# Performance work log

Measured on AMD Instinct MI355X. Metric: run time of the kernel, lower is better.

Reference implementation:

```python
import jax, jax.numpy as jnp
import numpy as np

B, LP, LH, D, H = 32, 1024, 1024, 256, 256

def setup_inputs() -> dict:
    key = jax.random.key(0)
    k1, k2, k3 = jax.random.split(key, 3)
    premises = jax.random.normal(k1, (B, LP, D), dtype=jnp.float32)
    hypotheses = jax.random.normal(k2, (B, LH, D), dtype=jnp.float32)
    W_F = jax.random.normal(k3, (D, H), dtype=jnp.float32) * (1.0 / np.sqrt(D))
    return {"premises": premises, "hypotheses": hypotheses, "W_F": W_F}

def reference(premises, hypotheses, W_F):
    # Tanh-projected features: F_p = tanh(P @ W_F), F_h = tanh(H @ W_F)
    F_p = jnp.tanh(jnp.einsum('bpd,dh->bph', premises, W_F))   # [B,LP,H]
    F_h = jnp.tanh(jnp.einsum('bqd,dh->bqh', hypotheses, W_F)) # [B,LH,H]
    # Alignment scores e_ij = F_p . F_h
    eijs = jnp.einsum('bph,bqh->bpq', F_p, F_h)                # [B,LP,LH]
    # betas: for each premise token, softmax over hypothesis tokens, weighted sum of hypotheses
    betas = jnp.einsum('bpq,bqd->bpd', jax.nn.softmax(eijs, axis=-1), hypotheses)  # [B,LP,D]
    # alphas: for each hypothesis token, softmax over premise tokens, weighted sum of premises
    alphas = jnp.einsum('bqp,bpd->bqd',
                        jax.nn.softmax(jnp.swapaxes(eijs, 1, 2), axis=-1),
                        premises)                                                   # [B,LH,D]
    return betas, alphas
```

## Files before the change

### kernel.cpp

```cpp
#include <hip/hip_runtime.h>

typedef _Float16 f16;
typedef __attribute__((ext_vector_type(4))) _Float16 f16x4;
typedef __attribute__((ext_vector_type(8))) _Float16 f16x8;
typedef __attribute__((ext_vector_type(4))) float f32x4;
typedef __attribute__((ext_vector_type(16))) float f32x16;
typedef unsigned int u32;

#define BB 32
#define LL 1024
#define DD 256

#define VMCNT(N) asm volatile("s_waitcnt vmcnt(" #N ")" ::: "memory")
#define LGKMCNT0 asm volatile("s_waitcnt lgkmcnt(0)" ::: "memory")

__device__ __forceinline__ void async_copy16(const f16* g, f16* l) {
  __builtin_amdgcn_global_load_lds(
      (const __attribute__((address_space(1))) u32*)(const void*)g,
      (__attribute__((address_space(3))) u32*)(void*)l, 16, 0, 0);
}

__device__ __forceinline__ u32 pack_pkrtz(float a, float b) {
  auto pk = __builtin_amdgcn_cvt_pkrtz(a, b);
  u32 w;
  __builtin_memcpy(&w, &pk, 4);
  return w;
}

__global__ __launch_bounds__(256) void transpose_to_f16(
    const float* __restrict__ X0, f16* __restrict__ Y0,
    const float* __restrict__ X1, f16* __restrict__ Y1,
    int L, int D, int nbPerInput) {
  __shared__ float T[64][68];
  const int tid = threadIdx.x;
  int bz = blockIdx.z;
  const float* X = X0;
  f16* Y = Y0;
  int b = bz;
  if (bz >= nbPerInput) { X = X1; Y = Y1; b = bz - nbPerInput; }
  const int l0 = blockIdx.x * 64, d0 = blockIdx.y * 64;
  const size_t baseX = (size_t)b * L * D;
#pragma unroll
  for (int pass = 0; pass < 4; ++pass) {
    int r = (tid >> 4) + pass * 16;
    int c = (tid & 15) * 4;
    float4 v = *(const float4*)&X[baseX + (size_t)(l0 + r) * D + d0 + c];
    *(float4*)&T[r][c] = v;
  }
  __syncthreads();
  const size_t baseY = (size_t)b * D * L;
#pragma unroll
  for (int pass = 0; pass < 2; ++pass) {
    int dr = (tid >> 3) + pass * 32;
    int lc = (tid & 7) * 8;
    f16x8 o;
#pragma unroll
    for (int j = 0; j < 8; ++j) o[j] = (f16)T[lc + j][dr];
    *(f16x8*)&Y[baseY + (size_t)(d0 + dr) * L + l0 + lc] = o;
  }
}

__global__ __launch_bounds__(256, 2) void proj_mfma(
    const float* __restrict__ Pin, const float* __restrict__ Hin,
    const f16* __restrict__ Wt, f16* __restrict__ Fp, f16* __restrict__ Fh,
    f16* __restrict__ Vtp, f16* __restrict__ Vth) {
  __shared__ f16 As[64][258];
  __shared__ f16 Wts[64][258];
  const int tid = threadIdx.x;
  const int wv = tid >> 6, lane = tid & 63;
  const int l32 = lane & 31, half = lane >> 5;
  const int wm = wv >> 1, wn = wv & 1;
  const float* A = blockIdx.z ? Hin : Pin;
  f16* F = blockIdx.z ? Fh : Fp;
  f16* VtO = blockIdx.z ? Vth : Vtp;
  const int m0 = blockIdx.x * 64;

  {
    const int r = tid >> 4;
    const int c4 = (tid & 15) * 4;
#pragma unroll
    for (int p = 0; p < 4; ++p)
#pragma unroll
      for (int ch = 0; ch < 4; ++ch) {
        float4 v =
            *(const float4*)&A[(size_t)(m0 + r + p * 16) * 256 + ch * 64 + c4];
        f16x4 h4;
        h4[0] = (f16)v.x; h4[1] = (f16)v.y; h4[2] = (f16)v.z; h4[3] = (f16)v.w;
        *(f16x4*)&As[r + p * 16][ch * 64 + c4] = h4;
      }
  }
  __syncthreads();

  f16x8 af[16];
#pragma unroll
  for (int ks = 0; ks < 16; ++ks)
    af[ks] = *(const f16x8*)&As[wm * 32 + l32][ks * 16 + half * 8];

  {
    const int dd = tid & 63, lg = tid >> 6;
    const int bI = m0 >> 10, l_base = m0 & 1023;
#pragma unroll
    for (int kc = 0; kc < 4; ++kc) {
      f16* vrow =
          VtO + (size_t)bI * DD * LL + (size_t)(kc * 64 + dd) * LL + l_base;
#pragma unroll
      for (int part = 0; part < 2; ++part) {
        int lo = lg * 16 + part * 8;
        f16x8 ov;
#pragma unroll
        for (int j = 0; j < 8; ++j) ov[j] = As[lo + j][kc * 64 + dd];
        *(f16x8*)&vrow[lo] = ov;
      }
    }
  }

  for (int nc = 0; nc < 4; ++nc) {
    __syncthreads();
#pragma unroll
    for (int pass = 0; pass < 8; ++pass) {
      int row = (tid >> 5) + pass * 8;
      int chunk = tid & 31;
      *(f16x8*)&Wts[row][chunk * 8] =
          *(const f16x8*)&Wt[(size_t)(nc * 64 + row) * 256 + chunk * 8];
    }
    __syncthreads();
    f32x16 acc = (f32x16)(0.f);
#pragma unroll
    for (int ks = 0; ks < 16; ++ks) {
      f16x8 wf = *(const f16x8*)&Wts[wn * 32 + l32][ks * 16 + half * 8];
      acc = __builtin_amdgcn_mfma_f32_32x32x16_f16(af[ks], wf, acc, 0, 0, 0);
    }
#pragma unroll
    for (int r = 0; r < 16; ++r) {
      float x = acc[r];
      float e = __expf(2.f * x);
      float th = 1.f - 2.f / (e + 1.f);
      F[(size_t)(m0 + wm * 32 + (r & 3) + 8 * (r >> 2) + 4 * half) * 256 +
        nc * 64 + wn * 32 + l32] = (f16)th;
    }
  }
}

__global__ __launch_bounds__(256, 2) void flash_mfma(
    const f16* __restrict__ Fpm, const f16* __restrict__ Fhm,
    const f16* __restrict__ Vth, const f16* __restrict__ Vtp,
    float* __restrict__ Out) {
  __shared__ f16 Kf[2][16][512];
  __shared__ f16 Vf[2][16][512];

  const int tid = threadIdx.x;
  const int wv = tid >> 6, lane = tid & 63;
  const int l32 = lane & 31, half = lane >> 5;

  const f16* Fq = Fpm;
  const f16* Fk = Fhm;
  const f16* Vt = Vth;
  float* O = Out;
  if (blockIdx.y) { Fq = Fhm; Fk = Fpm; Vt = Vtp; O = Out + (size_t)BB * LL * DD; }

  const int x = blockIdx.x;
  const int b = ((x & 7) << 2) | (x >> 6);
  const int p0 = ((x >> 3) & 7) * 128 + wv * 32;
  const int p = p0 + l32;

  const f16* Fq_b = Fq + (size_t)b * LL * DD;
  const f16* Fk_b = Fk + (size_t)b * LL * DD;
  const f16* Vt_b = Vt + (size_t)b * DD * LL;

  f16x8 qf[16];
  {
    const f16* qrow = Fq_b + (size_t)p * DD + half * 8;
#pragma unroll
    for (int s = 0; s < 16; ++s) qf[s] = *(const f16x8*)&qrow[s * 16];
  }

  float m_run = -1e30f, l_run = 0.f;
  f32x16 o[8];
#pragma unroll
  for (int t = 0; t < 8; ++t) o[t] = (f32x16)(0.f);

  auto stage = [&](int buf, int q0) {
#pragma unroll
    for (int i = 0; i < 4; ++i) {
      int s = wv * 4 + i;
      async_copy16(Fk_b + (size_t)(q0 + l32) * DD + s * 16 + half * 8,
                   &Kf[buf][s][0]);
    }
#pragma unroll
    for (int i = 0; i < 4; ++i) {
      int v = wv * 4 + i;
      int t = v >> 1, h = v & 1;
      async_copy16(Vt_b + (size_t)(t * 32 + l32) * LL + q0 + h * 16 + half * 8,
                   &Vf[buf][v][0]);
    }
  };

  auto tile_compute = [&](int cur) {
    f32x16 S = (f32x16)(0.f);
    __builtin_amdgcn_s_setprio(1);
#pragma unroll
    for (int s = 0; s < 16; ++s) {
      f16x8 kf = *(const f16x8*)&Kf[cur][s][lane * 8];
      S = __builtin_amdgcn_mfma_f32_32x32x16_f16(kf, qf[s], S, 0, 0, 0);
    }
    __builtin_amdgcn_s_setprio(0);

    float mt = S[0];
#pragma unroll
    for (int r = 1; r < 16; ++r) mt = fmaxf(mt, S[r]);
    mt = fmaxf(mt, __shfl_xor(mt, 32, 64));

    const bool keep = __all((int)(mt - m_run <= 8.0f)) != 0;
    const float mn = keep ? m_run : fmaxf(m_run, mt);
    float pe[16];
    float ts = 0.f;
#pragma unroll
    for (int r = 0; r < 16; ++r) {
      pe[r] = __expf(S[r] - mn);
      ts += pe[r];
    }
    ts += __shfl_xor(ts, 32, 64);
    if (!keep) {
      const float alpha = __expf(m_run - mn);
      l_run *= alpha;
      m_run = mn;
#pragma unroll
      for (int t = 0; t < 8; ++t)
#pragma unroll
        for (int r = 0; r < 16; ++r) o[t][r] *= alpha;
    }
    l_run += ts;

    u32 pw[8];
#pragma unroll
    for (int i = 0; i < 8; ++i) pw[i] = pack_pkrtz(pe[2 * i], pe[2 * i + 1]);
    u32 rc[4];
    {
      u32 s0 = half ? pw[0] : pw[2];
      u32 s1 = half ? pw[1] : pw[3];
      u32 s2 = half ? pw[4] : pw[6];
      u32 s3 = half ? pw[5] : pw[7];
      rc[0] = (u32)__shfl_xor((int)s0, 32, 64);
      rc[1] = (u32)__shfl_xor((int)s1, 32, 64);
      rc[2] = (u32)__shfl_xor((int)s2, 32, 64);
      rc[3] = (u32)__shfl_xor((int)s3, 32, 64);
    }
    f16x8 pf[2];
#pragma unroll
    for (int h = 0; h < 2; ++h) {
      u32 tmp[4];
      tmp[0] = half ? rc[2 * h] : pw[4 * h];
      tmp[1] = half ? rc[2 * h + 1] : pw[4 * h + 1];
      tmp[2] = half ? pw[4 * h + 2] : rc[2 * h];
      tmp[3] = half ? pw[4 * h + 3] : rc[2 * h + 1];
      __builtin_memcpy(&pf[h], tmp, 16);
    }

    __builtin_amdgcn_s_setprio(1);
#pragma unroll
    for (int t = 0; t < 8; ++t) {
      f16x8 v0 = *(const f16x8*)&Vf[cur][t * 2][lane * 8];
      o[t] = __builtin_amdgcn_mfma_f32_32x32x16_f16(v0, pf[0], o[t], 0, 0, 0);
      f16x8 v1 = *(const f16x8*)&Vf[cur][t * 2 + 1][lane * 8];
      o[t] = __builtin_amdgcn_mfma_f32_32x32x16_f16(v1, pf[1], o[t], 0, 0, 0);
    }
    __builtin_amdgcn_s_setprio(0);
  };

  stage(0, 0);
  int cur = 0;
  for (int it = 0; it < 31; ++it) {
    stage(cur ^ 1, (it + 1) * 32);
    VMCNT(8);
    __builtin_amdgcn_sched_barrier(0);
    __builtin_amdgcn_s_barrier();
    tile_compute(cur);
    __builtin_amdgcn_s_barrier();
    cur ^= 1;
  }
  VMCNT(0);
  __builtin_amdgcn_sched_barrier(0);
  __builtin_amdgcn_s_barrier();
  tile_compute(cur);
  __syncthreads();

  const float inv = 1.f / l_run;
  float* Tw = (float*)&Kf[0][0][0] + wv * (32 * 36);
  float* Ob = O + (size_t)b * LL * DD;
#pragma unroll
  for (int t = 0; t < 8; ++t) {
#pragma unroll
    for (int g = 0; g < 4; ++g) {
      int C = 2 * g + half;
      f32x4 v;
      v[0] = o[t][4 * g + 0] * inv;
      v[1] = o[t][4 * g + 1] * inv;
      v[2] = o[t][4 * g + 2] * inv;
      v[3] = o[t][4 * g + 3] * inv;
      *(f32x4*)&Tw[l32 * 36 + C * 4] = v;
    }
    LGKMCNT0;
#pragma unroll
    for (int pass = 0; pass < 4; ++pass) {
      int row = pass * 8 + (lane >> 3);
      int Cr = lane & 7;
      f32x4 v = *(const f32x4*)&Tw[row * 36 + Cr * 4];
      *(f32x4*)&Ob[(size_t)(p0 + row) * DD + t * 32 + Cr * 4] = v;
    }
    LGKMCNT0;
  }
}

extern "C" void kernel_launch(void* const* d_in, const int* in_sizes, int n_in,
                              void* d_out, int out_size, void* d_ws,
                              size_t ws_size, hipStream_t stream) {
  const float* premises = (const float*)d_in[0];
  const float* hypotheses = (const float*)d_in[1];
  const float* W = (const float*)d_in[2];
  float* out = (float*)d_out;

  const size_t MF = (size_t)BB * LL * DD;
  f16* Fp = (f16*)d_ws;
  f16* Fh = Fp + MF;
  f16* Vth = Fh + MF;
  f16* Vtp = Vth + MF;
  f16* Wt = (f16*)((char*)d_out + (size_t)out_size * 4 - 256 * 256 * 2);

  transpose_to_f16<<<dim3(4, 4, 1), 256, 0, stream>>>(W, Wt, W, Wt, 256, 256, 1);
  proj_mfma<<<dim3(512, 1, 2), 256, 0, stream>>>(premises, hypotheses, Wt, Fp,
                                                 Fh, Vtp, Vth);
  flash_mfma<<<dim3(256, 2), 256, 0, stream>>>(Fp, Fh, Vth, Vtp, out);
}
```

Measured before the change: 227.1 us.

## Pre-swizzle projected features and tiled V layout for contiguous async loads

The projection kernel now writes F rows with an XOR swizzle through shared memory. It writes V transposed into per-32-token tiles of 256x32, so the flash kernel can stage whole contiguous 16-byte lanes with global_load_lds and read them bank-conflict-free using matching XOR indices. W is read directly from global memory instead of being staged in LDS, which frees shared memory so occupancy can rise to 3 blocks. The QK product is split into two independent accumulators to shorten the MFMA dependency chain. The costs are extra XOR index arithmetic, uncached global reads of W per wave, and a dependency on both kernels agreeing on the swizzle.

```diff
diff --git a/kernel.cpp b/kernel.cpp
--- a/kernel.cpp
+++ b/kernel.cpp
@@ -60,12 +60,11 @@
   }
 }
 
-__global__ __launch_bounds__(256, 2) void proj_mfma(
+__global__ __launch_bounds__(256, 3) void proj_mfma(
     const float* __restrict__ Pin, const float* __restrict__ Hin,
     const f16* __restrict__ Wt, f16* __restrict__ Fp, f16* __restrict__ Fh,
     f16* __restrict__ Vtp, f16* __restrict__ Vth) {
-  __shared__ f16 As[64][258];
-  __shared__ f16 Wts[64][258];
+  __shared__ f16 As[64][264];
   const int tid = threadIdx.x;
   const int wv = tid >> 6, lane = tid & 63;
   const int l32 = lane & 31, half = lane >> 5;
@@ -79,14 +78,14 @@
     const int r = tid >> 4;
     const int c4 = (tid & 15) * 4;
 #pragma unroll
-    for (int p = 0; p < 4; ++p)
+    for (int pp = 0; pp < 4; ++pp)
 #pragma unroll
       for (int ch = 0; ch < 4; ++ch) {
         float4 v =
-            *(const float4*)&A[(size_t)(m0 + r + p * 16) * 256 + ch * 64 + c4];
+            *(const float4*)&A[(size_t)(m0 + r + pp * 16) * 256 + ch * 64 + c4];
         f16x4 h4;
         h4[0] = (f16)v.x; h4[1] = (f16)v.y; h4[2] = (f16)v.z; h4[3] = (f16)v.w;
-        *(f16x4*)&As[r + p * 16][ch * 64 + c4] = h4;
+        *(f16x4*)&As[r + pp * 16][ch * 64 + c4] = h4;
       }
   }
   __syncthreads();
@@ -97,47 +96,50 @@
     af[ks] = *(const f16x8*)&As[wm * 32 + l32][ks * 16 + half * 8];
 
   {
-    const int dd = tid & 63, lg = tid >> 6;
-    const int bI = m0 >> 10, l_base = m0 & 1023;
-#pragma unroll
-    for (int kc = 0; kc < 4; ++kc) {
-      f16* vrow =
-          VtO + (size_t)bI * DD * LL + (size_t)(kc * 64 + dd) * LL + l_base;
-#pragma unroll
-      for (int part = 0; part < 2; ++part) {
-        int lo = lg * 16 + part * 8;
-        f16x8 ov;
-#pragma unroll
-        for (int j = 0; j < 8; ++j) ov[j] = As[lo + j][kc * 64 + dd];
-        *(f16x8*)&vrow[lo] = ov;
-      }
-    }
-  }
-
+    const int bI = m0 >> 10;
+    const int T = ((m0 & 1023) >> 5) + (wv & 1);
+    const int dg = (wv >> 1) * 128;
+    const int jp = lane & 3;
+    const int j = jp ^ ((lane >> 3) & 3);
+    const int rloc = (wv & 1) * 32 + j * 8;
+#pragma unroll
+    for (int e = 0; e < 8; ++e) {
+      int d = dg + e * 16 + (lane >> 2);
+      f16x8 ov;
+#pragma unroll
+      for (int jj = 0; jj < 8; ++jj) ov[jj] = As[rloc + jj][d];
+      *(f16x8*)&VtO[((size_t)(bI * 32 + T) * 256 + d) * 32 + jp * 8] = ov;
+    }
+  }
+  __syncthreads();
+
+#pragma unroll
   for (int nc = 0; nc < 4; ++nc) {
-    __syncthreads();
-#pragma unroll
-    for (int pass = 0; pass < 8; ++pass) {
-      int row = (tid >> 5) + pass * 8;
-      int chunk = tid & 31;
-      *(f16x8*)&Wts[row][chunk * 8] =
-          *(const f16x8*)&Wt[(size_t)(nc * 64 + row) * 256 + chunk * 8];
-    }
-    __syncthreads();
     f32x16 acc = (f32x16)(0.f);
 #pragma unroll
     for (int ks = 0; ks < 16; ++ks) {
-      f16x8 wf = *(const f16x8*)&Wts[wn * 32 + l32][ks * 16 + half * 8];
+      f16x8 wf = *(const f16x8*)&Wt[(size_t)(nc * 64 + wn * 32 + l32) * 256 +
+                                    ks * 16 + half * 8];
       acc = __builtin_amdgcn_mfma_f32_32x32x16_f16(af[ks], wf, acc, 0, 0, 0);
     }
 #pragma unroll
     for (int r = 0; r < 16; ++r) {
-      float x = acc[r];
-      float e = __expf(2.f * x);
-      float th = 1.f - 2.f / (e + 1.f);
-      F[(size_t)(m0 + wm * 32 + (r & 3) + 8 * (r >> 2) + 4 * half) * 256 +
-        nc * 64 + wn * 32 + l32] = (f16)th;
-    }
+      float xv = acc[r];
+      float e2 = __expf(2.f * xv);
+      float th = 1.f - 2.f / (e2 + 1.f);
+      As[wm * 32 + (r & 3) + 8 * (r >> 2) + 4 * half]
+        [nc * 64 + wn * 32 + l32] = (f16)th;
+    }
+  }
+  __syncthreads();
+
+#pragma unroll
+  for (int e = 0; e < 8; ++e) {
+    int lm = wv * 16 + e * 2 + (lane >> 5);
+    int cp = lane & 31;
+    int c = cp ^ (lm & 15);
+    f16x8 ov = *(const f16x8*)&As[lm][c * 8];
+    *(f16x8*)&F[(size_t)(m0 + lm) * 256 + cp * 8] = ov;
   }
 }
 
@@ -145,8 +147,8 @@
     const f16* __restrict__ Fpm, const f16* __restrict__ Fhm,
     const f16* __restrict__ Vth, const f16* __restrict__ Vtp,
     float* __restrict__ Out) {
-  __shared__ f16 Kf[2][16][512];
-  __shared__ f16 Vf[2][16][512];
+  __shared__ f16 Kb[2][8192];
+  __shared__ f16 Vb[2][8192];
 
   const int tid = threadIdx.x;
   const int wv = tid >> 6, lane = tid & 63;
@@ -165,13 +167,15 @@
 
   const f16* Fq_b = Fq + (size_t)b * LL * DD;
   const f16* Fk_b = Fk + (size_t)b * LL * DD;
-  const f16* Vt_b = Vt + (size_t)b * DD * LL;
+  const f16* Vt_b = Vt + (size_t)b * LL * DD;
 
   f16x8 qf[16];
   {
-    const f16* qrow = Fq_b + (size_t)p * DD + half * 8;
-#pragma unroll
-    for (int s = 0; s < 16; ++s) qf[s] = *(const f16x8*)&qrow[s * 16];
+    const int qsw = p & 15;
+#pragma unroll
+    for (int s = 0; s < 16; ++s)
+      qf[s] = *(const f16x8*)&Fq_b[(size_t)p * DD +
+                                   (((2 * s + half) ^ qsw) << 3)];
   }
 
   float m_run = -1e30f, l_run = 0.f;
@@ -179,31 +183,40 @@
 #pragma unroll
   for (int t = 0; t < 8; ++t) o[t] = (f32x16)(0.f);
 
-  auto stage = [&](int buf, int q0) {
-#pragma unroll
-    for (int i = 0; i < 4; ++i) {
-      int s = wv * 4 + i;
-      async_copy16(Fk_b + (size_t)(q0 + l32) * DD + s * 16 + half * 8,
-                   &Kf[buf][s][0]);
-    }
-#pragma unroll
-    for (int i = 0; i < 4; ++i) {
-      int v = wv * 4 + i;
-      int t = v >> 1, h = v & 1;
-      async_copy16(Vt_b + (size_t)(t * 32 + l32) * LL + q0 + h * 16 + half * 8,
-                   &Vf[buf][v][0]);
+  const int ksw = l32 & 15;
+  const int vsw = (l32 >> 1) & 3;
+
+  auto stage = [&](int buf, int T) {
+#pragma unroll
+    for (int ii = 0; ii < 4; ++ii) {
+      int i = wv * 4 + ii;
+      async_copy16(Fk_b + (size_t)(T * 32 + 2 * i) * DD + lane * 8,
+                   &Kb[buf][i * 512]);
+    }
+#pragma unroll
+    for (int ii = 0; ii < 4; ++ii) {
+      int i = wv * 4 + ii;
+      async_copy16(Vt_b + (size_t)T * 8192 + i * 512 + lane * 8,
+                   &Vb[buf][i * 512]);
     }
   };
 
   auto tile_compute = [&](int cur) {
-    f32x16 S = (f32x16)(0.f);
+    f32x16 S0 = (f32x16)(0.f), S1 = (f32x16)(0.f);
     __builtin_amdgcn_s_setprio(1);
 #pragma unroll
-    for (int s = 0; s < 16; ++s) {
-      f16x8 kf = *(const f16x8*)&Kf[cur][s][lane * 8];
-      S = __builtin_amdgcn_mfma_f32_32x32x16_f16(kf, qf[s], S, 0, 0, 0);
+    for (int s = 0; s < 16; s += 2) {
+      f16x8 k0 = *(const f16x8*)&Kb[cur][(l32 << 8) +
+                                         (((2 * s + half) ^ ksw) << 3)];
+      S0 = __builtin_amdgcn_mfma_f32_32x32x16_f16(k0, qf[s], S0, 0, 0, 0);
+      f16x8 k1 = *(const f16x8*)&Kb[cur][(l32 << 8) +
+                                         (((2 * s + 2 + half) ^ ksw) << 3)];
+      S1 = __builtin_amdgcn_mfma_f32_32x32x16_f16(k1, qf[s + 1], S1, 0, 0, 0);
     }
     __builtin_amdgcn_s_setprio(0);
+    f32x16 S;
+#pragma unroll
+    for (int r = 0; r < 16; ++r) S[r] = S0[r] + S1[r];
 
     float mt = S[0];
 #pragma unroll
@@ -259,9 +272,10 @@
     __builtin_amdgcn_s_setprio(1);
 #pragma unroll
     for (int t = 0; t < 8; ++t) {
-      f16x8 v0 = *(const f16x8*)&Vf[cur][t * 2][lane * 8];
+      int vrow = (t * 32 + l32) << 5;
+      f16x8 v0 = *(const f16x8*)&Vb[cur][vrow + ((half ^ vsw) << 3)];
       o[t] = __builtin_amdgcn_mfma_f32_32x32x16_f16(v0, pf[0], o[t], 0, 0, 0);
-      f16x8 v1 = *(const f16x8*)&Vf[cur][t * 2 + 1][lane * 8];
+      f16x8 v1 = *(const f16x8*)&Vb[cur][vrow + (((2 + half) ^ vsw) << 3)];
       o[t] = __builtin_amdgcn_mfma_f32_32x32x16_f16(v1, pf[1], o[t], 0, 0, 0);
     }
     __builtin_amdgcn_s_setprio(0);
@@ -270,7 +284,7 @@
   stage(0, 0);
   int cur = 0;
   for (int it = 0; it < 31; ++it) {
-    stage(cur ^ 1, (it + 1) * 32);
+    stage(cur ^ 1, it + 1);
     VMCNT(8);
     __builtin_amdgcn_sched_barrier(0);
     __builtin_amdgcn_s_barrier();
@@ -285,7 +299,7 @@
   __syncthreads();
 
   const float inv = 1.f / l_run;
-  float* Tw = (float*)&Kf[0][0][0] + wv * (32 * 36);
+  float* Tw = (float*)&Kb[0][0] + wv * (32 * 36);
   float* Ob = O + (size_t)b * LL * DD;
 #pragma unroll
   for (int t = 0; t < 8; ++t) {
```

Result: slower. 241.4 us (+6.3%).
